# Kernel tuning notes

Measured on AMD Instinct MI355X. Metric: run time of the kernel, lower is better.

## Reference

```python
import jax, jax.numpy as jnp
import numpy as np

# ---- static config (matches init_kwargs) ----
N_BANDS = 8
WIN = 2048
R = 0.5
SR = 16000
STRIDE = WIN - int(R * WIN)  # 1024
Q = 0.707  # torchaudio default Q for high/lowpass_biquad


def _hp_coeffs(cutoff):
    w0 = 2.0 * np.pi * cutoff / SR
    alpha = np.sin(w0) / (2.0 * Q)
    cw = np.cos(w0)
    b0 = (1.0 + cw) / 2.0
    b1 = -(1.0 + cw)
    b2 = (1.0 + cw) / 2.0
    a0 = 1.0 + alpha
    a1 = -2.0 * cw
    a2 = 1.0 - alpha
    return tuple(np.float32(v / a0) for v in (b0, b1, b2, a1, a2))


def _lp_coeffs(cutoff):
    w0 = 2.0 * np.pi * cutoff / SR
    alpha = np.sin(w0) / (2.0 * Q)
    cw = np.cos(w0)
    b0 = (1.0 - cw) / 2.0
    b1 = 1.0 - cw
    b2 = (1.0 - cw) / 2.0
    a0 = 1.0 + alpha
    a1 = -2.0 * cw
    a2 = 1.0 - alpha
    return tuple(np.float32(v / a0) for v in (b0, b1, b2, a1, a2))


# fixed weighting biquad: b=(1,-2,1), a=(1,-1.8,0.81), already a0-normalized
_WEIGHT = (np.float32(1.0), np.float32(-2.0), np.float32(1.0), np.float32(-1.8), np.float32(0.81))


def _biquad(x, coefs):
    """Direct-form I biquad along the last axis; zero initial conditions (matches torchaudio lfilter)."""
    b0, b1, b2, a1, a2 = coefs
    shape = x.shape
    flat = x.reshape(-1, shape[-1])  # [rows, T]
    z = jnp.zeros((flat.shape[0],), dtype=x.dtype)

    def step(carry, xt):
        x1, x2, y1, y2 = carry
        y = b0 * xt + b1 * x1 + b2 * x2 - a1 * y1 - a2 * y2
        return (xt, x1, y, y1), y

    _, ys = jax.lax.scan(step, (z, z, z, z), flat.T)  # ys: [T, rows]
    return jnp.moveaxis(ys, 0, 1).reshape(shape)


def _unfold(x):
    """x: [batch, T] -> [batch, n_seg, WIN] with stride STRIDE (torch.unfold semantics)."""
    T = x.shape[1]
    n_seg = (T - WIN) // STRIDE + 1
    idx = jnp.arange(n_seg)[:, None] * STRIDE + jnp.arange(WIN)[None, :]
    return x[:, idx]


def _loudness(segments):
    weighted = _biquad(segments, _WEIGHT)
    energy = jnp.mean(weighted * weighted, axis=-1)  # [batch, n_seg]
    return 10.0 * jnp.log10(energy + 1e-8)


def _forward(signal, watermark):
    losses = []
    for i in range(N_BANDS):
        low_cut = i * SR / (2 * N_BANDS)
        high_cut = (i + 1) * SR / (2 * N_BANDS)
        hp = _hp_coeffs(low_cut)
        lp = _lp_coeffs(high_cut)
        band_sig = _biquad(_biquad(signal, hp), lp)
        band_wm = _biquad(_biquad(watermark, hp), lp)
        loud_sig = _loudness(_unfold(band_sig))
        loud_wm = _loudness(_unfold(band_wm))
        losses.append(jnp.mean(jnp.abs(loud_wm - loud_sig)))
    return jnp.mean(jnp.stack(losses))


def setup_inputs() -> dict:
    key = jax.random.key(0)
    k1, k2 = jax.random.split(key)
    signal = jax.random.normal(k1, (32, 160000), dtype=jnp.float32)
    watermark = jax.random.normal(k2, (32, 160000), dtype=jnp.float32)
    return {"signal": signal, "watermark": watermark}


def reference(signal, watermark):
    return _forward(signal, watermark)
```

## Files before the change

kernel.cpp:

```cpp
#include <hip/hip_runtime.h>
#include <cmath>

#ifndef M_PI
#define M_PI 3.14159265358979323846
#endif

#define T_LEN   160000
#define NSEG    155
#define ROWS    32
#define NBANDS  8

#define CHUNK   256
#define NSUB    4
#define NQ      16
#define QPC     64
#define NCHUNK  624
#define TOT_IT  (NCHUNK + 2)
#define LOUD_FLOATS (NBANDS * 2 * ROWS * NSEG)

struct AllCoefs {
    float h[NBANDS][5];
    float l[NBANDS][5];
};

__device__ __forceinline__ void barrier_lds_only() {
    asm volatile("s_waitcnt lgkmcnt(0)\n\ts_barrier" ::: "memory");
}

__global__ __launch_bounds__(192, 1)
void tf_pipe3_kernel(const float* __restrict__ sig, const float* __restrict__ wm,
                     float* __restrict__ loud, AllCoefs C) {
    __shared__ float I1[2][CHUNK * 32];
    __shared__ float I2[2][CHUNK * 32];

    const int band = blockIdx.x;
    const int src  = blockIdx.y;
    const int tid  = threadIdx.x;
    const int wid  = tid >> 6;
    const int lane = tid & 63;
    const int ch   = lane & 31;

    const float hb0 = C.h[band][0], hb1 = C.h[band][1], hb2 = C.h[band][2];
    const float hna1 = -C.h[band][3], hna2 = -C.h[band][4];
    const float lb0 = C.l[band][0], lb1 = C.l[band][1], lb2 = C.l[band][2];
    const float lna1 = -C.l[band][3], lna2 = -C.l[band][4];
    const float NA1 =  1.79999995231628417969f;
    const float NA2 = -0.810000002384185791f;

    const float* __restrict__ xrow = (src ? wm : sig) + (size_t)ch * T_LEN;
    const float4* __restrict__ xq  = (const float4*)xrow;

    float x1 = 0.f, x2 = 0.f, y1 = 0.f, y2 = 0.f, acc = 0.f;

    float4 pfA[NQ], pfB[NQ];
    if (wid == 0 && lane < 32) {
        #pragma unroll
        for (int i = 0; i < NQ; ++i) pfA[i] = xq[i];
    }

#define HP1(xx, oo)                                                          \
    {  float s1 = __fmaf_rn(hb0, xx, __fmul_rn(hb1, x1));                    \
       float s2 = __fmaf_rn(hb2, x2, s1); x2 = x1; x1 = xx;                  \
       float s3 = __fmaf_rn(hna1, y1, s2);                                   \
       oo = __fmaf_rn(hna2, y2, s3); y2 = y1; y1 = oo; }

#define W0SUB(USE, FILL, cc, s, NEXTQ)                                       \
    {                                                                        \
        float4* __restrict__ ob = (float4*)I1[(cc) & 1];                     \
        _Pragma("unroll")                                                    \
        for (int i = 0; i < NQ; ++i) {                                       \
            float4 v = USE[i];                                               \
            FILL[i] = xq[(NEXTQ) + i];                                       \
            float4 o;                                                        \
            HP1(v.x, o.x) HP1(v.y, o.y) HP1(v.z, o.z) HP1(v.w, o.w)          \
            ob[((s) * NQ + i) * 32 + ch] = o;                                \
        }                                                                    \
    }

    for (int iter = 0; iter < TOT_IT; ++iter) {
        if (wid == 0) {
            if (iter < NCHUNK && lane < 32) {
                const int c = iter;
                const int q0 = c * QPC;
                W0SUB(pfA, pfB, c, 0, q0 + 1 * NQ)
                W0SUB(pfB, pfA, c, 1, q0 + 2 * NQ)
                W0SUB(pfA, pfB, c, 2, q0 + 3 * NQ)
                W0SUB(pfB, pfA, c, 3, q0 + 4 * NQ)
            }
        } else if (wid == 1) {
            if (iter >= 1 && iter <= NCHUNK && lane < 32) {
                const int c = iter - 1;
                const float4* __restrict__ ib = (const float4*)I1[c & 1];
                float4* __restrict__ ob = (float4*)I2[c & 1];
                #pragma unroll
                for (int s = 0; s < NSUB; ++s) {
                    float4 v[NQ];
                    #pragma unroll
                    for (int i = 0; i < NQ; ++i) v[i] = ib[(s * NQ + i) * 32 + ch];
                    #pragma unroll
                    for (int i = 0; i < NQ; ++i) {
                        float4 o;
                        #define LP1(xx, oo) \
                            { float s1 = __fmaf_rn(lb0, xx, __fmul_rn(lb1, x1)); \
                              float s2 = __fmaf_rn(lb2, x2, s1); x2 = x1; x1 = xx; \
                              float s3 = __fmaf_rn(lna1, y1, s2); \
                              oo = __fmaf_rn(lna2, y2, s3); y2 = y1; y1 = oo; }
                        LP1(v[i].x, o.x) LP1(v[i].y, o.y) LP1(v[i].z, o.z) LP1(v[i].w, o.w)
                        #undef LP1
                        ob[(s * NQ + i) * 32 + ch] = o;
                    }
                }
            }
        } else {
            if (iter >= 2) {
                const int c = iter - 2;
                const bool evenHalf = (lane < 32);
                const float4* __restrict__ ib = (const float4*)I2[c & 1];
                #pragma unroll
                for (int s = 0; s < NSUB; ++s) {
                    const int u = c * NSUB + s;
                    const int m32 = u & 31;
                    if ((m32 == (evenHalf ? 0 : 16)) && (u >> 4) < NSEG) {
                        x1 = 0.f; x2 = 0.f; y1 = 0.f; y2 = 0.f; acc = 0.f;
                    }
                    float4 v[NQ];
                    #pragma unroll
                    for (int i = 0; i < NQ; ++i) v[i] = ib[(s * NQ + i) * 32 + ch];
                    #pragma unroll
                    for (int i = 0; i < NQ; ++i) {
                        float s1, s2, s3, yy;
                        #define WSTEP(xx) \
                            s1 = __fmaf_rn(-2.0f, x1, xx); \
                            s2 = __fadd_rn(s1, x2); \
                            s3 = __fmaf_rn(NA1, y1, s2); \
                            yy = __fmaf_rn(NA2, y2, s3); \
                            x2 = x1; x1 = xx; y2 = y1; y1 = yy; \
                            acc = __fmaf_rn(yy, yy, acc);
                        WSTEP(v[i].x) WSTEP(v[i].y) WSTEP(v[i].z) WSTEP(v[i].w)
                        #undef WSTEP
                    }
                    const int endm = evenHalf ? 31 : 15;
                    if (m32 == endm && u >= 31) {
                        const int j = (u - 31) >> 4;
                        float e = __fmul_rn(acc, 0.00048828125f);
                        loud[((size_t)((band * 2 + src) * ROWS + ch)) * NSEG + j] =
                            __fmul_rn(10.0f, log10f(__fadd_rn(e, 1e-8f)));
                    }
                }
            }
        }
        barrier_lds_only();
    }
#undef W0SUB
#undef HP1
}

__global__ __launch_bounds__(256)
void tf_reduce_kernel(const float* __restrict__ loud, float* __restrict__ out) {
    __shared__ double sh[256];
    const int per_band = ROWS * NSEG;
    const int npairs   = NBANDS * per_band;
    double s = 0.0;
    for (int idx = threadIdx.x; idx < npairs; idx += 256) {
        int band = idx / per_band;
        int rs   = idx - band * per_band;
        float a = loud[(size_t)(band * 2 + 0) * per_band + rs];
        float b = loud[(size_t)(band * 2 + 1) * per_band + rs];
        s += fabs((double)b - (double)a);
    }
    sh[threadIdx.x] = s;
    __syncthreads();
    for (int off = 128; off > 0; off >>= 1) {
        if (threadIdx.x < off) sh[threadIdx.x] += sh[threadIdx.x + off];
        __syncthreads();
    }
    if (threadIdx.x == 0) out[0] = (float)(sh[0] / (double)npairs);
}

static void mk_hp(double cutoff, float* o) {
    const double w0    = 2.0 * M_PI * cutoff / 16000.0;
    const double alpha = sin(w0) / (2.0 * 0.707);
    const double cw    = cos(w0);
    const double b0 = (1.0 + cw) / 2.0;
    const double b1 = -(1.0 + cw);
    const double b2 = (1.0 + cw) / 2.0;
    const double a0 = 1.0 + alpha;
    const double a1 = -2.0 * cw;
    const double a2 = 1.0 - alpha;
    o[0] = (float)(b0 / a0); o[1] = (float)(b1 / a0); o[2] = (float)(b2 / a0);
    o[3] = (float)(a1 / a0); o[4] = (float)(a2 / a0);
}

static void mk_lp(double cutoff, float* o) {
    const double w0    = 2.0 * M_PI * cutoff / 16000.0;
    const double alpha = sin(w0) / (2.0 * 0.707);
    const double cw    = cos(w0);
    const double b0 = (1.0 - cw) / 2.0;
    const double b1 = 1.0 - cw;
    const double b2 = (1.0 - cw) / 2.0;
    const double a0 = 1.0 + alpha;
    const double a1 = -2.0 * cw;
    const double a2 = 1.0 - alpha;
    o[0] = (float)(b0 / a0); o[1] = (float)(b1 / a0); o[2] = (float)(b2 / a0);
    o[3] = (float)(a1 / a0); o[4] = (float)(a2 / a0);
}

extern "C" void kernel_launch(void* const* d_in, const int* in_sizes, int n_in,
                              void* d_out, int out_size, void* d_ws, size_t ws_size,
                              hipStream_t stream) {
    const float* sig = (const float*)d_in[0];
    const float* wm  = (const float*)d_in[1];
    float* loud = (float*)d_ws;

    AllCoefs C;
    for (int i = 0; i < NBANDS; ++i) {
        mk_hp(1000.0 * (double)i,       C.h[i]);
        mk_lp(1000.0 * (double)(i + 1), C.l[i]);
    }

    tf_pipe3_kernel<<<dim3(NBANDS, 2), 192, 0, stream>>>(sig, wm, loud, C);
    tf_reduce_kernel<<<1, 256, 0, stream>>>(loud, (float*)d_out);
}
```

Baseline: 2.191 ms.

## Split biquad chain into six-wave pipeline through global-memory ring buffers

Adds a new kernel in which each of six wavefronts handles one stage of the filter chain: HP FIR, HP recursion, LP FIR, LP recursion, weighting FIR, and weighting recursion with energy accumulation. Stages hand data on through double-buffered global workspace rings instead of LDS, using 512-sample chunks and software-prefetched float4 loads. The goal is to shorten each wave's serial dependency chain by running the stages concurrently. In exchange it adds global-memory traffic and per-chunk barriers with vmcnt waits, and it falls back to the old kernel when the workspace is too small.

```diff
diff --git a/kernel.cpp b/kernel.cpp
--- a/kernel.cpp
+++ b/kernel.cpp
@@ -9,6 +9,11 @@
 #define NSEG    155
 #define ROWS    32
 #define NBANDS  8
+
+struct AllCoefs {
+    float h[NBANDS][5];
+    float l[NBANDS][5];
+};
 
 #define CHUNK   256
 #define NSUB    4
@@ -17,11 +22,6 @@
 #define NCHUNK  624
 #define TOT_IT  (NCHUNK + 2)
 #define LOUD_FLOATS (NBANDS * 2 * ROWS * NSEG)
-
-struct AllCoefs {
-    float h[NBANDS][5];
-    float l[NBANDS][5];
-};
 
 __device__ __forceinline__ void barrier_lds_only() {
     asm volatile("s_waitcnt lgkmcnt(0)\n\ts_barrier" ::: "memory");
@@ -153,6 +153,202 @@
     }
 #undef W0SUB
 #undef HP1
+}
+
+#define CH6     512
+#define QPC6    128
+#define NCH6    312
+#define TOT6    (NCH6 + 5)
+#define LOUD_F4 19840
+#define SLOT32  4096
+#define SLOT64  8192
+#define R32Q    (2 * SLOT32)
+#define R64Q    (2 * SLOT64)
+#define WS_NEED6 ((size_t)(LOUD_F4 + 64 * R32Q + 16 * R64Q) * 16)
+
+__device__ __forceinline__ void bar_vm0() {
+    asm volatile("s_waitcnt vmcnt(0)\n\ts_barrier" ::: "memory");
+}
+
+#define FIR3(B0, B1, B2, xx, oo) { \
+    float s1_ = __fmaf_rn(B0, xx, __fmul_rn(B1, x1)); \
+    oo = __fmaf_rn(B2, x2, s1_); x2 = x1; x1 = xx; }
+
+#define REC2(A1, A2, ff, oo) { \
+    float s3_ = __fmaf_rn(A1, y1, ff); \
+    oo = __fmaf_rn(A2, y2, s3_); y2 = y1; y1 = oo; }
+
+#define FIRW(xx, oo) { \
+    float s1_ = __fmaf_rn(-2.0f, x1, xx); \
+    oo = __fadd_rn(s1_, x2); x2 = x1; x1 = xx; }
+
+#define RECW(ff) { \
+    float s3_ = __fmaf_rn(NA1, y1, ff); \
+    float yy_ = __fmaf_rn(NA2, y2, s3_); \
+    y2 = y1; y1 = yy_; acc = __fmaf_rn(yy_, yy_, acc); }
+
+#define PIPE_BODY(IBQ, OBQ, STEP4)                                        \
+    {                                                                     \
+        _Pragma("unroll")                                                 \
+        for (int i = 0; i < 16; ++i) pfA[i] = IBQ(i);                     \
+        _Pragma("nounroll")                                               \
+        for (int sp = 0; sp < 4; ++sp) {                                  \
+            const int qA = sp * 32;                                       \
+            _Pragma("unroll")                                             \
+            for (int i = 0; i < 16; ++i) {                                \
+                float4 v = pfA[i];                                        \
+                pfB[i] = IBQ(qA + 16 + i);                                \
+                float4 o; STEP4(v, o);                                    \
+                OBQ(qA + i, o);                                           \
+            }                                                             \
+            _Pragma("unroll")                                             \
+            for (int i = 0; i < 16; ++i) {                                \
+                float4 v = pfB[i];                                        \
+                if (sp < 3) pfA[i] = IBQ(qA + 32 + i);                    \
+                float4 o; STEP4(v, o);                                    \
+                OBQ(qA + 16 + i, o);                                      \
+            }                                                             \
+        }                                                                 \
+    }
+
+__global__ __launch_bounds__(384, 1)
+void tf_pipe6_kernel(const float* __restrict__ sig, const float* __restrict__ wm,
+                     float* __restrict__ ws, AllCoefs C) {
+    const int band = blockIdx.x;
+    const int src  = blockIdx.y;
+    const int blk  = src * NBANDS + band;
+    const int tid  = threadIdx.x;
+    const int wid  = tid >> 6;
+    const int lane = tid & 63;
+    const int ch   = lane & 31;
+
+    float*  loud = ws;
+    float4* ring = (float4*)ws + LOUD_F4;
+    float4* fhp  = ring               + (size_t)blk * R32Q;
+    float4* yhp  = ring + 16 * R32Q   + (size_t)blk * R32Q;
+    float4* flp  = ring + 32 * R32Q   + (size_t)blk * R32Q;
+    float4* ylp  = ring + 48 * R32Q   + (size_t)blk * R32Q;
+    float4* fw   = ring + 64 * R32Q   + (size_t)blk * R64Q;
+
+    const float hb0 = C.h[band][0], hb1 = C.h[band][1], hb2 = C.h[band][2];
+    const float hna1 = -C.h[band][3], hna2 = -C.h[band][4];
+    const float lb0 = C.l[band][0], lb1 = C.l[band][1], lb2 = C.l[band][2];
+    const float lna1 = -C.l[band][3], lna2 = -C.l[band][4];
+    const float NA1 =  1.79999995231628417969f;
+    const float NA2 = -0.810000002384185791f;
+
+    const float* __restrict__ xrow = (src ? wm : sig) + (size_t)ch * T_LEN;
+    const float4* __restrict__ xq  = (const float4*)xrow;
+
+    float x1 = 0.f, x2 = 0.f, y1 = 0.f, y2 = 0.f, acc = 0.f;
+    float4 pfA[16], pfB[16];
+
+    if (wid == 0 && lane < 32) {
+        #pragma unroll
+        for (int i = 0; i < 16; ++i) pfA[i] = xq[i];
+    }
+
+    for (int it = 0; it < TOT6; ++it) {
+        if (wid == 0) {
+            const int c = it;
+            if (c < NCH6 && lane < 32) {
+                const int gq0 = c * QPC6;
+                float4* __restrict__ ob = fhp + (c & 1) * SLOT32;
+                #pragma nounroll
+                for (int sp = 0; sp < 4; ++sp) {
+                    const int qA = sp * 32;
+                    #pragma unroll
+                    for (int i = 0; i < 16; ++i) {
+                        float4 v = pfA[i];
+                        pfB[i] = xq[gq0 + qA + 16 + i];
+                        float4 o;
+                        FIR3(hb0, hb1, hb2, v.x, o.x) FIR3(hb0, hb1, hb2, v.y, o.y)
+                        FIR3(hb0, hb1, hb2, v.z, o.z) FIR3(hb0, hb1, hb2, v.w, o.w)
+                        ob[(qA + i) * 32 + ch] = o;
+                    }
+                    #pragma unroll
+                    for (int i = 0; i < 16; ++i) {
+                        float4 v = pfB[i];
+                        if (sp < 3) pfA[i] = xq[gq0 + qA + 32 + i];
+                        float4 o;
+                        FIR3(hb0, hb1, hb2, v.x, o.x) FIR3(hb0, hb1, hb2, v.y, o.y)
+                        FIR3(hb0, hb1, hb2, v.z, o.z) FIR3(hb0, hb1, hb2, v.w, o.w)
+                        ob[(qA + 16 + i) * 32 + ch] = o;
+                    }
+                }
+                __builtin_amdgcn_sched_barrier(0);
+                #pragma unroll
+                for (int i = 0; i < 16; ++i) pfA[i] = xq[gq0 + QPC6 + i];
+            }
+            asm volatile("s_waitcnt vmcnt(16)\n\ts_barrier" ::: "memory");
+        } else if (wid == 1) {
+            const int c = it - 1;
+            if (c >= 0 && c < NCH6 && lane < 32) {
+                const float4* __restrict__ ib = fhp + (c & 1) * SLOT32;
+                float4* __restrict__ ob = yhp + (c & 1) * SLOT32;
+                #define IBQ1(q)    ib[(q) * 32 + ch]
+                #define OBQ1(q, o) ob[(q) * 32 + ch] = (o)
+                #define STEP1(v, o) { REC2(hna1, hna2, v.x, o.x) REC2(hna1, hna2, v.y, o.y) \
+                                      REC2(hna1, hna2, v.z, o.z) REC2(hna1, hna2, v.w, o.w) }
+                PIPE_BODY(IBQ1, OBQ1, STEP1)
+            }
+            bar_vm0();
+        } else if (wid == 2) {
+            const int c = it - 2;
+            if (c >= 0 && c < NCH6 && lane < 32) {
+                const float4* __restrict__ ib = yhp + (c & 1) * SLOT32;
+                float4* __restrict__ ob = flp + (c & 1) * SLOT32;
+                #define IBQ2(q)    ib[(q) * 32 + ch]
+                #define OBQ2(q, o) ob[(q) * 32 + ch] = (o)
+                #define STEP2(v, o) { FIR3(lb0, lb1, lb2, v.x, o.x) FIR3(lb0, lb1, lb2, v.y, o.y) \
+                                      FIR3(lb0, lb1, lb2, v.z, o.z) FIR3(lb0, lb1, lb2, v.w, o.w) }
+                PIPE_BODY(IBQ2, OBQ2, STEP2)
+            }
+            bar_vm0();
+        } else if (wid == 3) {
+            const int c = it - 3;
+            if (c >= 0 && c < NCH6 && lane < 32) {
+                const float4* __restrict__ ib = flp + (c & 1) * SLOT32;
+                float4* __restrict__ ob = ylp + (c & 1) * SLOT32;
+                #define IBQ3(q)    ib[(q) * 32 + ch]
+                #define OBQ3(q, o) ob[(q) * 32 + ch] = (o)
+                #define STEP3(v, o) { REC2(lna1, lna2, v.x, o.x) REC2(lna1, lna2, v.y, o.y) \
+                                      REC2(lna1, lna2, v.z, o.z) REC2(lna1, lna2, v.w, o.w) }
+                PIPE_BODY(IBQ3, OBQ3, STEP3)
+            }
+            bar_vm0();
+        } else if (wid == 4) {
+            const int c = it - 4;
+            if (c >= 0 && c < NCH6) {
+                if ((c & 3) == (lane < 32 ? 0 : 2)) { x1 = 0.f; x2 = 0.f; }
+                const float4* __restrict__ ib = ylp + (c & 1) * SLOT32;
+                float4* __restrict__ ob = fw + (c & 1) * SLOT64;
+                #define IBQ4(q)    ib[(q) * 32 + ch]
+                #define OBQ4(q, o) ob[(q) * 64 + lane] = (o)
+                #define STEP4W(v, o) { FIRW(v.x, o.x) FIRW(v.y, o.y) FIRW(v.z, o.z) FIRW(v.w, o.w) }
+                PIPE_BODY(IBQ4, OBQ4, STEP4W)
+            }
+            bar_vm0();
+        } else {
+            const int c = it - 5;
+            if (c >= 0 && c < NCH6) {
+                const bool ev = (lane < 32);
+                if ((c & 3) == (ev ? 0 : 2)) { y1 = 0.f; y2 = 0.f; acc = 0.f; }
+                const float4* __restrict__ ib = fw + (c & 1) * SLOT64;
+                #define IBQ5(q)    ib[(q) * 64 + lane]
+                #define OBQ5(q, o) (void)(o)
+                #define STEP5(v, o) { RECW(v.x) RECW(v.y) RECW(v.z) RECW(v.w) (void)o; }
+                PIPE_BODY(IBQ5, OBQ5, STEP5)
+                if (c >= 3 && (c & 3) == (ev ? 3 : 1)) {
+                    const int j = (c - 3) >> 1;
+                    float e = __fmul_rn(acc, 0.00048828125f);
+                    loud[((size_t)((band * 2 + src) * ROWS + ch)) * NSEG + j] =
+                        __fmul_rn(10.0f, log10f(__fadd_rn(e, 1e-8f)));
+                }
+            }
+            bar_vm0();
+        }
+    }
 }
 
 __global__ __launch_bounds__(256)
@@ -210,7 +406,6 @@
                               hipStream_t stream) {
     const float* sig = (const float*)d_in[0];
     const float* wm  = (const float*)d_in[1];
-    float* loud = (float*)d_ws;
 
     AllCoefs C;
     for (int i = 0; i < NBANDS; ++i) {
@@ -218,6 +413,12 @@
         mk_lp(1000.0 * (double)(i + 1), C.l[i]);
     }
 
-    tf_pipe3_kernel<<<dim3(NBANDS, 2), 192, 0, stream>>>(sig, wm, loud, C);
-    tf_reduce_kernel<<<1, 256, 0, stream>>>(loud, (float*)d_out);
-}
+    if (ws_size >= WS_NEED6) {
+        tf_pipe6_kernel<<<dim3(NBANDS, 2), 384, 0, stream>>>(
+            sig, wm, (float*)d_ws, C);
+    } else {
+        tf_pipe3_kernel<<<dim3(NBANDS, 2), 192, 0, stream>>>(
+            sig, wm, (float*)d_ws, C);
+    }
+    tf_reduce_kernel<<<1, 256, 0, stream>>>((const float*)d_ws, (float*)d_out);
+}
```

Result: slower. 5.301 ms (+142.0%).

## Pack signal and watermark into one wave and triple-buffer LDS in place

Applied to the files above, without the earlier changes.

Each band now runs in a single 256-thread block instead of two 192-thread blocks. Lanes 0-31 filter the signal and lanes 32-63 the watermark, so the highpass and lowpass waves use all 64 lanes. Two weighting waves split the even and odd overlapping segments between them. A three-slot LDS ring replaces the separate I1/I2 double buffers, with the lowpass stage writing its output back into the same slot, and the chunk size drops to 192 samples. This halves the block count and doubles lane use per wave, at the cost of more pipeline barriers, since there are more, smaller chunks.

```diff
diff --git a/kernel.cpp b/kernel.cpp
--- a/kernel.cpp
+++ b/kernel.cpp
@@ -10,11 +10,11 @@
 #define ROWS    32
 #define NBANDS  8
 
-#define CHUNK   256
-#define NSUB    4
+#define CHUNK   192
+#define NSUB    3
 #define NQ      16
-#define QPC     64
-#define NCHUNK  624
+#define QPC     48
+#define NCHUNK  832
 #define TOT_IT  (NCHUNK + 2)
 #define LOUD_FLOATS (NBANDS * 2 * ROWS * NSEG)
 
@@ -27,18 +27,17 @@
     asm volatile("s_waitcnt lgkmcnt(0)\n\ts_barrier" ::: "memory");
 }
 
-__global__ __launch_bounds__(192, 1)
-void tf_pipe3_kernel(const float* __restrict__ sig, const float* __restrict__ wm,
+__global__ __launch_bounds__(256, 1)
+void tf_pipe4_kernel(const float* __restrict__ sig, const float* __restrict__ wm,
                      float* __restrict__ loud, AllCoefs C) {
-    __shared__ float I1[2][CHUNK * 32];
-    __shared__ float I2[2][CHUNK * 32];
+    __shared__ float4 I[3][QPC * 64];
 
     const int band = blockIdx.x;
-    const int src  = blockIdx.y;
     const int tid  = threadIdx.x;
     const int wid  = tid >> 6;
     const int lane = tid & 63;
-    const int ch   = lane & 31;
+    const int row  = lane & 31;
+    const int src  = lane >> 5;
 
     const float hb0 = C.h[band][0], hb1 = C.h[band][1], hb2 = C.h[band][2];
     const float hna1 = -C.h[band][3], hna2 = -C.h[band][4];
@@ -47,13 +46,13 @@
     const float NA1 =  1.79999995231628417969f;
     const float NA2 = -0.810000002384185791f;
 
-    const float* __restrict__ xrow = (src ? wm : sig) + (size_t)ch * T_LEN;
+    const float* __restrict__ xrow = (src ? wm : sig) + (size_t)row * T_LEN;
     const float4* __restrict__ xq  = (const float4*)xrow;
 
     float x1 = 0.f, x2 = 0.f, y1 = 0.f, y2 = 0.f, acc = 0.f;
 
     float4 pfA[NQ], pfB[NQ];
-    if (wid == 0 && lane < 32) {
+    if (wid == 0) {
         #pragma unroll
         for (int i = 0; i < NQ; ++i) pfA[i] = xq[i];
     }
@@ -64,94 +63,101 @@
        float s3 = __fmaf_rn(hna1, y1, s2);                                   \
        oo = __fmaf_rn(hna2, y2, s3); y2 = y1; y1 = oo; }
 
-#define W0SUB(USE, FILL, cc, s, NEXTQ)                                       \
+#define LP1(xx, oo)                                                          \
+    {  float s1 = __fmaf_rn(lb0, xx, __fmul_rn(lb1, x1));                    \
+       float s2 = __fmaf_rn(lb2, x2, s1); x2 = x1; x1 = xx;                  \
+       float s3 = __fmaf_rn(lna1, y1, s2);                                   \
+       oo = __fmaf_rn(lna2, y2, s3); y2 = y1; y1 = oo; }
+
+#define W0SUB(USE, FILL, S, NEXTQ)                                           \
     {                                                                        \
-        float4* __restrict__ ob = (float4*)I1[(cc) & 1];                     \
         _Pragma("unroll")                                                    \
         for (int i = 0; i < NQ; ++i) {                                       \
             float4 v = USE[i];                                               \
             FILL[i] = xq[(NEXTQ) + i];                                       \
             float4 o;                                                        \
             HP1(v.x, o.x) HP1(v.y, o.y) HP1(v.z, o.z) HP1(v.w, o.w)          \
-            ob[((s) * NQ + i) * 32 + ch] = o;                                \
-        }                                                                    \
-    }
+            ob[((S) * NQ + i) * 64 + lane] = o;                              \
+        }                                                                    \
+    }
+
+#define W1SUB(S)                                                             \
+    {                                                                        \
+        float4 v[NQ];                                                        \
+        _Pragma("unroll")                                                    \
+        for (int i = 0; i < NQ; ++i) v[i] = b[((S) * NQ + i) * 64 + lane];   \
+        _Pragma("unroll")                                                    \
+        for (int i = 0; i < NQ; ++i) {                                       \
+            float4 o;                                                        \
+            LP1(v[i].x, o.x) LP1(v[i].y, o.y) LP1(v[i].z, o.z) LP1(v[i].w, o.w) \
+            b[((S) * NQ + i) * 64 + lane] = o;                               \
+        }                                                                    \
+    }
+
+#define WGSUB(S)                                                             \
+    {                                                                        \
+        const int u = c * NSUB + (S);            \
+        const int m32 = u & 31;                                              \
+        if ((m32 == (EV ? 0 : 16)) && (u >> 4) < NSEG) {                     \
+            x1 = 0.f; x2 = 0.f; y1 = 0.f; y2 = 0.f; acc = 0.f;               \
+        }                                                                    \
+        float4 v[NQ];                                                        \
+        _Pragma("unroll")                                                    \
+        for (int i = 0; i < NQ; ++i) v[i] = b[((S) * NQ + i) * 64 + lane];   \
+        _Pragma("unroll")                                                    \
+        for (int i = 0; i < NQ; ++i) {                                       \
+            float s1, s2, s3, yy;                                            \
+             \
+            WSTEP(v[i].x) WSTEP(v[i].y) WSTEP(v[i].z) WSTEP(v[i].w)          \
+        }                                                                    \
+        const int endm = EV ? 31 : 15;                                       \
+        if (m32 == endm && u >= 31) {                                        \
+            const int j = (u - 31) >> 4;                                     \
+            float e = __fmul_rn(acc, 0.00048828125f);       \
+            loud[((size_t)((band * 2 + src) * ROWS + row)) * NSEG + j] =     \
+                __fmul_rn(10.0f, log10f(__fadd_rn(e, 1e-8f)));               \
+        }                                                                    \
+    }
+
+#define WSTEP(xx) \
+    s1 = __fmaf_rn(-2.0f, x1, xx); \
+    s2 = __fadd_rn(s1, x2); \
+    s3 = __fmaf_rn(NA1, y1, s2); \
+    yy = __fmaf_rn(NA2, y2, s3); \
+    x2 = x1; x1 = xx; y2 = y1; y1 = yy; \
+    acc = __fmaf_rn(yy, yy, acc);
 
     for (int iter = 0; iter < TOT_IT; ++iter) {
         if (wid == 0) {
-            if (iter < NCHUNK && lane < 32) {
+            if (iter < NCHUNK) {
                 const int c = iter;
                 const int q0 = c * QPC;
-                W0SUB(pfA, pfB, c, 0, q0 + 1 * NQ)
-                W0SUB(pfB, pfA, c, 1, q0 + 2 * NQ)
-                W0SUB(pfA, pfB, c, 2, q0 + 3 * NQ)
-                W0SUB(pfB, pfA, c, 3, q0 + 4 * NQ)
+                float4* __restrict__ ob = I[c % 3];
+                W0SUB(pfA, pfB, 0, q0 + 1 * NQ)
+                W0SUB(pfB, pfA, 1, q0 + 2 * NQ)
+                W0SUB(pfA, pfA, 2, q0 + 3 * NQ)
             }
         } else if (wid == 1) {
-            if (iter >= 1 && iter <= NCHUNK && lane < 32) {
-                const int c = iter - 1;
-                const float4* __restrict__ ib = (const float4*)I1[c & 1];
-                float4* __restrict__ ob = (float4*)I2[c & 1];
-                #pragma unroll
-                for (int s = 0; s < NSUB; ++s) {
-                    float4 v[NQ];
-                    #pragma unroll
-                    for (int i = 0; i < NQ; ++i) v[i] = ib[(s * NQ + i) * 32 + ch];
-                    #pragma unroll
-                    for (int i = 0; i < NQ; ++i) {
-                        float4 o;
-                        #define LP1(xx, oo) \
-                            { float s1 = __fmaf_rn(lb0, xx, __fmul_rn(lb1, x1)); \
-                              float s2 = __fmaf_rn(lb2, x2, s1); x2 = x1; x1 = xx; \
-                              float s3 = __fmaf_rn(lna1, y1, s2); \
-                              oo = __fmaf_rn(lna2, y2, s3); y2 = y1; y1 = oo; }
-                        LP1(v[i].x, o.x) LP1(v[i].y, o.y) LP1(v[i].z, o.z) LP1(v[i].w, o.w)
-                        #undef LP1
-                        ob[(s * NQ + i) * 32 + ch] = o;
-                    }
-                }
+            const int c = iter - 1;
+            if (c >= 0 && c < NCHUNK) {
+                float4* __restrict__ b = I[c % 3];
+                W1SUB(0) W1SUB(1) W1SUB(2)
             }
         } else {
-            if (iter >= 2) {
-                const int c = iter - 2;
-                const bool evenHalf = (lane < 32);
-                const float4* __restrict__ ib = (const float4*)I2[c & 1];
-                #pragma unroll
-                for (int s = 0; s < NSUB; ++s) {
-                    const int u = c * NSUB + s;
-                    const int m32 = u & 31;
-                    if ((m32 == (evenHalf ? 0 : 16)) && (u >> 4) < NSEG) {
-                        x1 = 0.f; x2 = 0.f; y1 = 0.f; y2 = 0.f; acc = 0.f;
-                    }
-                    float4 v[NQ];
-                    #pragma unroll
-                    for (int i = 0; i < NQ; ++i) v[i] = ib[(s * NQ + i) * 32 + ch];
-                    #pragma unroll
-                    for (int i = 0; i < NQ; ++i) {
-                        float s1, s2, s3, yy;
-                        #define WSTEP(xx) \
-                            s1 = __fmaf_rn(-2.0f, x1, xx); \
-                            s2 = __fadd_rn(s1, x2); \
-                            s3 = __fmaf_rn(NA1, y1, s2); \
-                            yy = __fmaf_rn(NA2, y2, s3); \
-                            x2 = x1; x1 = xx; y2 = y1; y1 = yy; \
-                            acc = __fmaf_rn(yy, yy, acc);
-                        WSTEP(v[i].x) WSTEP(v[i].y) WSTEP(v[i].z) WSTEP(v[i].w)
-                        #undef WSTEP
-                    }
-                    const int endm = evenHalf ? 31 : 15;
-                    if (m32 == endm && u >= 31) {
-                        const int j = (u - 31) >> 4;
-                        float e = __fmul_rn(acc, 0.00048828125f);
-                        loud[((size_t)((band * 2 + src) * ROWS + ch)) * NSEG + j] =
-                            __fmul_rn(10.0f, log10f(__fadd_rn(e, 1e-8f)));
-                    }
-                }
+            const bool EV = (wid == 2);
+            const int c = iter - 2;
+            if (c >= 0 && c < NCHUNK) {
+                const float4* __restrict__ b = I[c % 3];
+                WGSUB(0) WGSUB(1) WGSUB(2)
             }
         }
         barrier_lds_only();
     }
+#undef WSTEP
+#undef WGSUB
+#undef W1SUB
 #undef W0SUB
+#undef LP1
 #undef HP1
 }
 
@@ -218,6 +224,6 @@
         mk_lp(1000.0 * (double)(i + 1), C.l[i]);
     }
 
-    tf_pipe3_kernel<<<dim3(NBANDS, 2), 192, 0, stream>>>(sig, wm, loud, C);
+    tf_pipe4_kernel<<<dim3(NBANDS), 256, 0, stream>>>(sig, wm, loud, C);
     tf_reduce_kernel<<<1, 256, 0, stream>>>(loud, (float*)d_out);
 }
```

Result: no change. 2.202 ms (+0.5%).
